# Kernel optimization log

Hardware: AMD Instinct MI355X
Metric: run time of the kernel (lower is better)

Reference implementation:

```python
import jax, jax.numpy as jnp
import numpy as np

EMBED_DIM = 1024
NUM_HEADS = 16
HEAD_DIM = EMBED_DIM // NUM_HEADS
B, S = 2, 2048


def setup_inputs() -> dict:
    key = jax.random.key(0)
    ks = jax.random.split(key, 11)
    sc = 1.0 / np.sqrt(EMBED_DIM)
    d = {
        'query': jax.random.normal(ks[0], (B, S, EMBED_DIM), jnp.float32),
        'key': jax.random.normal(ks[1], (B, S, EMBED_DIM), jnp.float32),
        'value': jax.random.normal(ks[2], (B, S, EMBED_DIM), jnp.float32),
        'Wq': jax.random.normal(ks[3], (EMBED_DIM, EMBED_DIM), jnp.float32) * sc,
        'bq': jnp.zeros((EMBED_DIM,), jnp.float32),
        'Wk': jax.random.normal(ks[4], (EMBED_DIM, EMBED_DIM), jnp.float32) * sc,
        'bk': jnp.zeros((EMBED_DIM,), jnp.float32),
        'Wv': jax.random.normal(ks[5], (EMBED_DIM, EMBED_DIM), jnp.float32) * sc,
        'bv': jnp.zeros((EMBED_DIM,), jnp.float32),
        'Wo': jax.random.normal(ks[6], (EMBED_DIM, EMBED_DIM), jnp.float32) * sc,
        'bo': jnp.zeros((EMBED_DIM,), jnp.float32),
    }
    return d


def reference(query, key, value, Wq, bq, Wk, bk, Wv, bv, Wo, bo):
    b, s, _ = query.shape
    scale = 1.0 / np.sqrt(HEAD_DIM)
    # projections: torch Linear is x @ W.T + b
    q = (query @ Wq.T + bq).reshape(b, s, NUM_HEADS, HEAD_DIM).transpose(0, 2, 1, 3)
    k = (key @ Wk.T + bk).reshape(b, s, NUM_HEADS, HEAD_DIM).transpose(0, 2, 1, 3)
    v = (value @ Wv.T + bv).reshape(b, s, NUM_HEADS, HEAD_DIM).transpose(0, 2, 1, 3)
    scores = jnp.einsum('bhqd,bhkd->bhqk', q, k) * scale  # [B,H,S,S]
    causal = jnp.triu(jnp.ones((s, s), bool), k=1)
    scores = jnp.where(causal, -jnp.inf, scores)
    attn = jax.nn.softmax(scores, axis=-1)
    out = jnp.einsum('bhqk,bhkd->bhqd', attn, v)
    out = out.transpose(0, 2, 1, 3).reshape(b, s, EMBED_DIM)
    out = out @ Wo.T + bo
    return out, attn
```

## Files before the change

### kernel.cpp

```cpp
#include <hip/hip_runtime.h>
#include <hip/hip_bf16.h>

#define BATCH  2
#define SEQ    2048
#define EMBED  1024
#define NHEADS 16
#define HDIM   64
#define SCALE  0.125f
#define S2     0.180336880f
#define MFIX   20.0f
#define PPITCH 72

typedef __attribute__((ext_vector_type(8))) short   short8;
typedef __attribute__((ext_vector_type(4))) float   floatx4;

#if __has_builtin(__builtin_amdgcn_exp2f)
#define EXP2(x) __builtin_amdgcn_exp2f(x)
#else
#define EXP2(x) exp2f(x)
#endif

#define GLOAD_LDS(g, l) __builtin_amdgcn_global_load_lds(                      \
    (const __attribute__((address_space(1))) void*)(const void*)(g),           \
    (__attribute__((address_space(3))) void*)(void*)(l), 16, 0, 0)

__device__ __forceinline__ float bf2f(unsigned short h) {
    union { unsigned int u; float f; } v; v.u = ((unsigned int)h) << 16; return v.f;
}
__device__ __forceinline__ unsigned short f2bf(float f) {
    union { float f; unsigned int u; } v; v.f = f;
    unsigned int r = v.u + 0x7FFF + ((v.u >> 16) & 1);
    return (unsigned short)(r >> 16);
}
__device__ __forceinline__ unsigned int pack2(float lo, float hi) {
    return (unsigned int)f2bf(lo) | ((unsigned int)f2bf(hi) << 16);
}

__device__ __forceinline__ void bar_lds() {
    __builtin_amdgcn_sched_barrier(0);
    asm volatile("s_waitcnt lgkmcnt(0)" ::: "memory");
    __builtin_amdgcn_s_barrier();
    __builtin_amdgcn_sched_barrier(0);
}

__global__ __launch_bounds__(256)
void cvt_bf16(const float* __restrict__ q,  const float* __restrict__ k,
              const float* __restrict__ v,  const float* __restrict__ wq,
              const float* __restrict__ wk, const float* __restrict__ wv,
              const float* __restrict__ wo,
              unsigned short* __restrict__ dq,  unsigned short* __restrict__ dk,
              unsigned short* __restrict__ dv,  unsigned short* __restrict__ dwq,
              unsigned short* __restrict__ dwk, unsigned short* __restrict__ dwv,
              unsigned short* __restrict__ dwo)
{
    const float* s; unsigned short* d; int n;
    switch (blockIdx.y) {
        case 0: s = q;  d = dq;  n = BATCH * SEQ * EMBED; break;
        case 1: s = k;  d = dk;  n = BATCH * SEQ * EMBED; break;
        case 2: s = v;  d = dv;  n = BATCH * SEQ * EMBED; break;
        case 3: s = wq; d = dwq; n = EMBED * EMBED; break;
        case 4: s = wk; d = dwk; n = EMBED * EMBED; break;
        case 5: s = wv; d = dwv; n = EMBED * EMBED; break;
        default: s = wo; d = dwo; n = EMBED * EMBED; break;
    }
    const int i = (blockIdx.x * 256 + threadIdx.x) * 8;
    if (i >= n) return;
    float4 f0 = ((const float4*)(s + i))[0];
    float4 f1 = ((const float4*)(s + i))[1];
    uint4 u = {pack2(f0.x, f0.y), pack2(f0.z, f0.w),
               pack2(f1.x, f1.y), pack2(f1.z, f1.w)};
    *(uint4*)(d + i) = u;
}

__device__ __forceinline__ void gemm_body(
    const unsigned short* __restrict__ A,
    const unsigned short* __restrict__ W,
    const float* __restrict__ bias,
    void* __restrict__ Cout, const int f32out,
    const int bx, const int by)
{
    constexpr int N = EMBED;
    constexpr int K = EMBED;

    __shared__ unsigned short As[128 * 64];
    __shared__ unsigned short Bs[128 * 64];

    const int t    = threadIdx.x;
    const int w    = t >> 6;
    const int lane = t & 63;
    const int lr   = lane & 15;
    const int quad = lane >> 4;
    const int wr   = w >> 1;
    const int wc   = w & 1;
    const int n0   = bx * 128;
    const int m0   = by * 128;

    size_t agoff[4], bgoff[4];
    #pragma unroll
    for (int i = 0; i < 4; ++i) {
        const int slot = i * 256 + t;
        const int row  = slot >> 3;
        const int g    = (slot & 7) ^ (row & 7);
        agoff[i] = (size_t)(m0 + row) * K + g * 8;
        bgoff[i] = (size_t)(n0 + row) * K + g * 8;
    }

    int aoff[4][2], boff[4][2];
    #pragma unroll
    for (int mb = 0; mb < 4; ++mb)
        #pragma unroll
        for (int s = 0; s < 2; ++s) {
            const int row = wr * 64 + mb * 16 + lr;
            aoff[mb][s] = row * 64 + (((s * 4 + quad) ^ (row & 7)) * 8);
        }
    #pragma unroll
    for (int nb = 0; nb < 4; ++nb)
        #pragma unroll
        for (int s = 0; s < 2; ++s) {
            const int row = wc * 64 + nb * 16 + lr;
            boff[nb][s] = row * 64 + (((s * 4 + quad) ^ (row & 7)) * 8);
        }

    floatx4 acc[4][4];
    #pragma unroll
    for (int mb = 0; mb < 4; ++mb)
        #pragma unroll
        for (int nb = 0; nb < 4; ++nb) acc[mb][nb] = (floatx4){0.f, 0.f, 0.f, 0.f};

    for (int k0 = 0; k0 < K; k0 += 64) {
        __syncthreads();
        #pragma unroll
        for (int i = 0; i < 4; ++i)
            GLOAD_LDS(A + agoff[i] + k0, &As[(i * 256 + w * 64) * 8]);
        #pragma unroll
        for (int i = 0; i < 4; ++i)
            GLOAD_LDS(W + bgoff[i] + k0, &Bs[(i * 256 + w * 64) * 8]);
        __syncthreads();

        #pragma unroll
        for (int s = 0; s < 2; ++s) {
            short8 av[4], bv[4];
            #pragma unroll
            for (int mb = 0; mb < 4; ++mb) av[mb] = *(const short8*)&As[aoff[mb][s]];
            #pragma unroll
            for (int nb = 0; nb < 4; ++nb) bv[nb] = *(const short8*)&Bs[boff[nb][s]];
            #pragma unroll
            for (int mb = 0; mb < 4; ++mb)
                #pragma unroll
                for (int nb = 0; nb < 4; ++nb)
                    acc[mb][nb] = __builtin_amdgcn_mfma_f32_16x16x32_bf16(av[mb], bv[nb], acc[mb][nb], 0, 0, 0);
        }
    }

    #pragma unroll
    for (int mb = 0; mb < 4; ++mb)
        #pragma unroll
        for (int nb = 0; nb < 4; ++nb) {
            const int col = n0 + wc * 64 + nb * 16 + lr;
            const float bv = bias[col];
            #pragma unroll
            for (int r = 0; r < 4; ++r) {
                const int row = m0 + wr * 64 + mb * 16 + quad * 4 + r;
                const float val = acc[mb][nb][r] + bv;
                if (f32out) ((float*)Cout)[(size_t)row * N + col] = val;
                else        ((unsigned short*)Cout)[(size_t)row * N + col] = f2bf(val);
            }
        }
}

__global__ __launch_bounds__(256)
void gemm_qkv(const unsigned short* __restrict__ xq, const unsigned short* __restrict__ xk,
              const unsigned short* __restrict__ xv,
              const unsigned short* __restrict__ wq, const unsigned short* __restrict__ wk,
              const unsigned short* __restrict__ wv,
              const float* __restrict__ bq, const float* __restrict__ bk,
              const float* __restrict__ bv,
              unsigned short* __restrict__ Qb, unsigned short* __restrict__ Kb,
              unsigned short* __restrict__ Vb)
{
    const unsigned short *A, *W; const float* bias; unsigned short* C;
    switch (blockIdx.z) {
        case 0:  A = xq; W = wq; bias = bq; C = Qb; break;
        case 1:  A = xk; W = wk; bias = bk; C = Kb; break;
        default: A = xv; W = wv; bias = bv; C = Vb; break;
    }
    gemm_body(A, W, bias, C, 0, blockIdx.x, blockIdx.y);
}

__global__ __launch_bounds__(256)
void gemm_out(const unsigned short* __restrict__ A, const unsigned short* __restrict__ W,
              const float* __restrict__ bias, float* __restrict__ Cout)
{
    gemm_body(A, W, bias, Cout, 1, blockIdx.x, blockIdx.y);
}

__global__ __launch_bounds__(256)
void attn_pass(const unsigned short* __restrict__ Qb,
               const unsigned short* __restrict__ Kb,
               const unsigned short* __restrict__ Vb,
               unsigned short* __restrict__ Pb,
               unsigned short* __restrict__ AO)
{
    __shared__ unsigned short Ks[2][64][PPITCH];
    __shared__ unsigned short Vt[2][64][PPITCH];
    __shared__ unsigned short Ps[64][PPITCH];
    __shared__ float          Linv[64];

    const int t    = threadIdx.x;
    const int w    = t >> 6;
    const int lane = t & 63;
    const int lr   = lane & 15;
    const int quad = lane >> 4;
    const int h    = blockIdx.y;
    const int b    = blockIdx.z;
    const int slot = (h >> 3) + 2 * b;
    const int qt   = (slot & 1) ? (SEQ / 64 - 1 - (int)blockIdx.x) : (int)blockIdx.x;
    const int q0   = qt * 64;
    const int srow = t >> 2;
    const int sseg = (t & 3) * 16;
    const int bh   = b * NHEADS + h;

    const size_t kvbase = (size_t)b * SEQ * EMBED + h * HDIM;

    const unsigned short* qrow = Qb + kvbase + (size_t)(q0 + w * 16 + lr) * EMBED + quad * 8;
    const short8 af0 = *(const short8*)(qrow);
    const short8 af1 = *(const short8*)(qrow + 32);

    const unsigned short* Krow = Kb + kvbase + (size_t)srow * EMBED + sseg;
    const unsigned short* Vrow = Vb + kvbase + (size_t)lane * EMBED;

    uint4 kA0, kA1, vA0, vA1;
    uint4 kB0, kB1, vB0, vB1;

    kA0 = ((const uint4*)Krow)[0];
    kA1 = ((const uint4*)Krow)[1];
    vA0 = *(const uint4*)(Vrow + w * 8);
    vA1 = *(const uint4*)(Vrow + (w + 4) * 8);
    *(uint4*)&Ks[0][srow][sseg]     = kA0;
    *(uint4*)&Ks[0][srow][sseg + 8] = kA1;
    {
        const unsigned short* p0 = (const unsigned short*)&vA0;
        const unsigned short* p1 = (const unsigned short*)&vA1;
        #pragma unroll
        for (int j = 0; j < 8; ++j) Vt[0][w * 8 + j][lane]       = p0[j];
        #pragma unroll
        for (int j = 0; j < 8; ++j) Vt[0][(w + 4) * 8 + j][lane] = p1[j];
    }
    if (qt > 0) {
        const unsigned short* kp = Krow + (size_t)64 * EMBED;
        kB0 = ((const uint4*)kp)[0];
        kB1 = ((const uint4*)kp)[1];
        vB0 = *(const uint4*)(Vrow + (size_t)64 * EMBED + w * 8);
        vB1 = *(const uint4*)(Vrow + (size_t)64 * EMBED + (w + 4) * 8);
    }
    bar_lds();

    float lsum[4];
    #pragma unroll
    for (int r = 0; r < 4; ++r) lsum[r] = 0.f;
    floatx4 of[4];
    #pragma unroll
    for (int i = 0; i < 4; ++i) of[i] = (floatx4){0.f, 0.f, 0.f, 0.f};

    unsigned short* pb_bh = Pb + (size_t)bh * SEQ * (SEQ * 2);
    const int rrow = lane >> 2;
    const int rseg = (lane & 3) * 16;

    for (int kt = 0; kt <= qt; ++kt) {
        const int c  = kt & 1;
        const int k0 = kt * 64;

        if (kt < qt) {
            if ((kt & 1) == 0) {
                *(uint4*)&Ks[c ^ 1][srow][sseg]     = kB0;
                *(uint4*)&Ks[c ^ 1][srow][sseg + 8] = kB1;
                const unsigned short* p0 = (const unsigned short*)&vB0;
                const unsigned short* p1 = (const unsigned short*)&vB1;
                #pragma unroll
                for (int j = 0; j < 8; ++j) Vt[c ^ 1][w * 8 + j][lane]       = p0[j];
                #pragma unroll
                for (int j = 0; j < 8; ++j) Vt[c ^ 1][(w + 4) * 8 + j][lane] = p1[j];
                if (kt + 2 <= qt) {
                    const unsigned short* kp = Krow + (size_t)(k0 + 128) * EMBED;
                    kA0 = ((const uint4*)kp)[0];
                    kA1 = ((const uint4*)kp)[1];
                    vA0 = *(const uint4*)(Vrow + (size_t)(k0 + 128) * EMBED + w * 8);
                    vA1 = *(const uint4*)(Vrow + (size_t)(k0 + 128) * EMBED + (w + 4) * 8);
                }
            } else {
                *(uint4*)&Ks[c ^ 1][srow][sseg]     = kA0;
                *(uint4*)&Ks[c ^ 1][srow][sseg + 8] = kA1;
                const unsigned short* p0 = (const unsigned short*)&vA0;
                const unsigned short* p1 = (const unsigned short*)&vA1;
                #pragma unroll
                for (int j = 0; j < 8; ++j) Vt[c ^ 1][w * 8 + j][lane]       = p0[j];
                #pragma unroll
                for (int j = 0; j < 8; ++j) Vt[c ^ 1][(w + 4) * 8 + j][lane] = p1[j];
                if (kt + 2 <= qt) {
                    const unsigned short* kp = Krow + (size_t)(k0 + 128) * EMBED;
                    kB0 = ((const uint4*)kp)[0];
                    kB1 = ((const uint4*)kp)[1];
                    vB0 = *(const uint4*)(Vrow + (size_t)(k0 + 128) * EMBED + w * 8);
                    vB1 = *(const uint4*)(Vrow + (size_t)(k0 + 128) * EMBED + (w + 4) * 8);
                }
            }
        }

        floatx4 sf[4];
        #pragma unroll
        for (int i = 0; i < 4; ++i) sf[i] = (floatx4){0.f, 0.f, 0.f, 0.f};
        #pragma unroll
        for (int nb = 0; nb < 4; ++nb) {
            short8 bf0 = *(const short8*)&Ks[c][nb * 16 + lr][quad * 8];
            sf[nb] = __builtin_amdgcn_mfma_f32_16x16x32_bf16(af0, bf0, sf[nb], 0, 0, 0);
        }
        #pragma unroll
        for (int nb = 0; nb < 4; ++nb) {
            short8 bf1 = *(const short8*)&Ks[c][nb * 16 + lr][32 + quad * 8];
            sf[nb] = __builtin_amdgcn_mfma_f32_16x16x32_bf16(af1, bf1, sf[nb], 0, 0, 0);
        }

        if (kt < qt) {
            #pragma unroll
            for (int nb = 0; nb < 4; ++nb)
                #pragma unroll
                for (int r = 0; r < 4; ++r) {
                    float p = EXP2(sf[nb][r] * S2 - MFIX);
                    lsum[r] += p;
                    Ps[w * 16 + quad * 4 + r][nb * 16 + lr] = f2bf(p);
                }
        } else {
            #pragma unroll
            for (int nb = 0; nb < 4; ++nb) {
                const int k = nb * 16 + lr;
                #pragma unroll
                for (int r = 0; r < 4; ++r) {
                    const int q = w * 16 + quad * 4 + r;
                    float p = 0.f;
                    if (k <= q) { p = EXP2(sf[nb][r] * S2 - MFIX); lsum[r] += p; }
                    Ps[w * 16 + quad * 4 + r][nb * 16 + lr] = f2bf(p);
                }
            }
        }

        {
            const unsigned short* ps = &Ps[w * 16 + rrow][rseg];
            unsigned short* op = pb_bh + (size_t)(q0 + w * 16 + rrow) * (SEQ * 2) + k0 + rseg;
            *(uint4*)op       = *(const uint4*)ps;
            *(uint4*)(op + 8) = *(const uint4*)(ps + 8);
        }

        #pragma unroll
        for (int ss = 0; ss < 2; ++ss) {
            short8 paf = *(const short8*)&Ps[w * 16 + lr][ss * 32 + quad * 8];
            #pragma unroll
            for (int nb = 0; nb < 4; ++nb) {
                short8 vf = *(const short8*)&Vt[c][nb * 16 + lr][ss * 32 + quad * 8];
                of[nb] = __builtin_amdgcn_mfma_f32_16x16x32_bf16(paf, vf, of[nb], 0, 0, 0);
            }
        }

        bar_lds();
    }

    float invl[4];
    #pragma unroll
    for (int r = 0; r < 4; ++r) {
        #pragma unroll
        for (int off = 1; off < 16; off <<= 1)
            lsum[r] += __shfl_xor(lsum[r], off, 64);
        invl[r] = 1.f / lsum[r];
    }
    if (lr == 0) {
        #pragma unroll
        for (int r = 0; r < 4; ++r)
            Linv[w * 16 + quad * 4 + r] = invl[r];
    }

    #pragma unroll
    for (int nb = 0; nb < 4; ++nb)
        #pragma unroll
        for (int r = 0; r < 4; ++r)
            Ps[w * 16 + quad * 4 + r][nb * 16 + lr] = f2bf(of[nb][r] * invl[r]);
    {
        unsigned short* ao = AO + (size_t)(b * SEQ + q0 + w * 16 + rrow) * EMBED + h * HDIM + rseg;
        *(uint4*)ao       = *(const uint4*)&Ps[w * 16 + rrow][rseg];
        *(uint4*)(ao + 8) = *(const uint4*)&Ps[w * 16 + rrow][rseg + 8];
    }

    __builtin_amdgcn_sched_barrier(0);
    asm volatile("s_waitcnt vmcnt(0) lgkmcnt(0)" ::: "memory");
    __builtin_amdgcn_sched_barrier(0);

    float* fb = ((float*)Pb) + (size_t)bh * SEQ * SEQ;
    const int qc = q0 + 64;
    for (int i = 0; i < 16; ++i) {
        const int q  = q0 + w * 16 + i;
        const float il = Linv[w * 16 + i];
        const unsigned short* src = pb_bh + (size_t)q * (SEQ * 2);
        float* dst = fb + (size_t)q * SEQ;

        uint4 rr[4];
        #pragma unroll
        for (int s = 0; s < 4; ++s) {
            const int cc = s * 512 + lane * 8;
            if (cc < qc) rr[s] = *(const uint4*)(src + cc);
        }
        #pragma unroll
        for (int s = 0; s < 4; ++s) {
            const int cc = s * 512 + lane * 8;
            if (cc < qc) {
                const unsigned short* u = (const unsigned short*)&rr[s];
                float4 f0 = {bf2f(u[0]) * il, bf2f(u[1]) * il, bf2f(u[2]) * il, bf2f(u[3]) * il};
                float4 f1 = {bf2f(u[4]) * il, bf2f(u[5]) * il, bf2f(u[6]) * il, bf2f(u[7]) * il};
                ((float4*)(dst + cc))[0] = f0;
                ((float4*)(dst + cc))[1] = f1;
            }
        }
    }
}

extern "C" void kernel_launch(void* const* d_in, const int* in_sizes, int n_in,
                              void* d_out, int out_size, void* d_ws, size_t ws_size,
                              hipStream_t stream)
{
    const float* query = (const float*)d_in[0];
    const float* key   = (const float*)d_in[1];
    const float* value = (const float*)d_in[2];
    const float* Wq    = (const float*)d_in[3];
    const float* bq    = (const float*)d_in[4];
    const float* Wk    = (const float*)d_in[5];
    const float* bk    = (const float*)d_in[6];
    const float* Wv    = (const float*)d_in[7];
    const float* bv    = (const float*)d_in[8];
    const float* Wo    = (const float*)d_in[9];
    const float* bo    = (const float*)d_in[10];

    float* out  = (float*)d_out;
    float* attn = out + (size_t)BATCH * SEQ * EMBED;

    const size_t tsz = (size_t)BATCH * SEQ * EMBED;
    const size_t wsz = (size_t)EMBED * EMBED;
    unsigned short* p = (unsigned short*)d_ws;
    unsigned short* xq  = p;  p += tsz;
    unsigned short* xk  = p;  p += tsz;
    unsigned short* xv  = p;  p += tsz;
    unsigned short* wq16 = p; p += wsz;
    unsigned short* wk16 = p; p += wsz;
    unsigned short* wv16 = p; p += wsz;
    unsigned short* wo16 = p; p += wsz;
    unsigned short* Qb  = p;  p += tsz;
    unsigned short* Kb  = p;  p += tsz;
    unsigned short* Vb  = p;  p += tsz;
    unsigned short* AO  = p;  p += tsz;

    const dim3 blk(256);

    cvt_bf16<<<dim3(2048, 7), blk, 0, stream>>>(query, key, value, Wq, Wk, Wv, Wo,
                                                xq, xk, xv, wq16, wk16, wv16, wo16);

    const dim3 gqkv(EMBED / 128, (BATCH * SEQ) / 128, 3);
    gemm_qkv<<<gqkv, blk, 0, stream>>>(xq, xk, xv, wq16, wk16, wv16,
                                       bq, bk, bv, Qb, Kb, Vb);

    attn_pass<<<dim3(SEQ / 64, NHEADS, BATCH), blk, 0, stream>>>(
        Qb, Kb, Vb, (unsigned short*)attn, AO);

    gemm_out<<<dim3(EMBED / 128, (BATCH * SEQ) / 128), blk, 0, stream>>>(AO, wo16, bo, out);
}
```

Before: 746.7 us.

## Recompute QK^T in a second pass to write normalized attn directly

Before, unnormalized bf16 probabilities were stored into the attn buffer during the flash loop, then read back, scaled by the row inverse sum and expanded to fp32. Now the first pass only accumulates row sums and the PV output. A second loop over K tiles recomputes the scores with MFMA and writes normalized fp32 probabilities straight to attn. This removes the bf16 scratch write and read-back round trip, at the cost of doubling the QK^T MFMA work and K tile loads. Upper-triangle entries are not written, so the code relies on attn being zeroed elsewhere.

```diff
diff --git a/kernel.cpp b/kernel.cpp
--- a/kernel.cpp
+++ b/kernel.cpp
@@ -198,13 +198,12 @@
 void attn_pass(const unsigned short* __restrict__ Qb,
                const unsigned short* __restrict__ Kb,
                const unsigned short* __restrict__ Vb,
-               unsigned short* __restrict__ Pb,
+               float* __restrict__ attn,
                unsigned short* __restrict__ AO)
 {
     __shared__ unsigned short Ks[2][64][PPITCH];
     __shared__ unsigned short Vt[2][64][PPITCH];
     __shared__ unsigned short Ps[64][PPITCH];
-    __shared__ float          Linv[64];
 
     const int t    = threadIdx.x;
     const int w    = t >> 6;
@@ -262,10 +261,6 @@
     #pragma unroll
     for (int i = 0; i < 4; ++i) of[i] = (floatx4){0.f, 0.f, 0.f, 0.f};
 
-    unsigned short* pb_bh = Pb + (size_t)bh * SEQ * (SEQ * 2);
-    const int rrow = lane >> 2;
-    const int rseg = (lane & 3) * 16;
-
     for (int kt = 0; kt <= qt; ++kt) {
         const int c  = kt & 1;
         const int k0 = kt * 64;
@@ -343,13 +338,6 @@
             }
         }
 
-        {
-            const unsigned short* ps = &Ps[w * 16 + rrow][rseg];
-            unsigned short* op = pb_bh + (size_t)(q0 + w * 16 + rrow) * (SEQ * 2) + k0 + rseg;
-            *(uint4*)op       = *(const uint4*)ps;
-            *(uint4*)(op + 8) = *(const uint4*)(ps + 8);
-        }
-
         #pragma unroll
         for (int ss = 0; ss < 2; ++ss) {
             short8 paf = *(const short8*)&Ps[w * 16 + lr][ss * 32 + quad * 8];
@@ -371,11 +359,6 @@
             lsum[r] += __shfl_xor(lsum[r], off, 64);
         invl[r] = 1.f / lsum[r];
     }
-    if (lr == 0) {
-        #pragma unroll
-        for (int r = 0; r < 4; ++r)
-            Linv[w * 16 + quad * 4 + r] = invl[r];
-    }
 
     #pragma unroll
     for (int nb = 0; nb < 4; ++nb)
@@ -383,40 +366,86 @@
         for (int r = 0; r < 4; ++r)
             Ps[w * 16 + quad * 4 + r][nb * 16 + lr] = f2bf(of[nb][r] * invl[r]);
     {
+        const int rrow = lane >> 2;
+        const int rseg = (lane & 3) * 16;
         unsigned short* ao = AO + (size_t)(b * SEQ + q0 + w * 16 + rrow) * EMBED + h * HDIM + rseg;
         *(uint4*)ao       = *(const uint4*)&Ps[w * 16 + rrow][rseg];
         *(uint4*)(ao + 8) = *(const uint4*)&Ps[w * 16 + rrow][rseg + 8];
     }
 
-    __builtin_amdgcn_sched_barrier(0);
-    asm volatile("s_waitcnt vmcnt(0) lgkmcnt(0)" ::: "memory");
-    __builtin_amdgcn_sched_barrier(0);
-
-    float* fb = ((float*)Pb) + (size_t)bh * SEQ * SEQ;
-    const int qc = q0 + 64;
-    for (int i = 0; i < 16; ++i) {
-        const int q  = q0 + w * 16 + i;
-        const float il = Linv[w * 16 + i];
-        const unsigned short* src = pb_bh + (size_t)q * (SEQ * 2);
-        float* dst = fb + (size_t)q * SEQ;
-
-        uint4 rr[4];
-        #pragma unroll
-        for (int s = 0; s < 4; ++s) {
-            const int cc = s * 512 + lane * 8;
-            if (cc < qc) rr[s] = *(const uint4*)(src + cc);
-        }
-        #pragma unroll
-        for (int s = 0; s < 4; ++s) {
-            const int cc = s * 512 + lane * 8;
-            if (cc < qc) {
-                const unsigned short* u = (const unsigned short*)&rr[s];
-                float4 f0 = {bf2f(u[0]) * il, bf2f(u[1]) * il, bf2f(u[2]) * il, bf2f(u[3]) * il};
-                float4 f1 = {bf2f(u[4]) * il, bf2f(u[5]) * il, bf2f(u[6]) * il, bf2f(u[7]) * il};
-                ((float4*)(dst + cc))[0] = f0;
-                ((float4*)(dst + cc))[1] = f1;
-            }
-        }
+    kA0 = ((const uint4*)Krow)[0];
+    kA1 = ((const uint4*)Krow)[1];
+    if (qt > 0) {
+        const unsigned short* kp = Krow + (size_t)64 * EMBED;
+        kB0 = ((const uint4*)kp)[0];
+        kB1 = ((const uint4*)kp)[1];
+    }
+    *(uint4*)&Ks[0][srow][sseg]     = kA0;
+    *(uint4*)&Ks[0][srow][sseg + 8] = kA1;
+    bar_lds();
+
+    float* fb = attn + (size_t)bh * SEQ * SEQ;
+    for (int kt = 0; kt <= qt; ++kt) {
+        const int c  = kt & 1;
+        const int k0 = kt * 64;
+
+        if (kt < qt) {
+            if ((kt & 1) == 0) {
+                *(uint4*)&Ks[c ^ 1][srow][sseg]     = kB0;
+                *(uint4*)&Ks[c ^ 1][srow][sseg + 8] = kB1;
+                if (kt + 2 <= qt) {
+                    const unsigned short* kp = Krow + (size_t)(k0 + 128) * EMBED;
+                    kA0 = ((const uint4*)kp)[0];
+                    kA1 = ((const uint4*)kp)[1];
+                }
+            } else {
+                *(uint4*)&Ks[c ^ 1][srow][sseg]     = kA0;
+                *(uint4*)&Ks[c ^ 1][srow][sseg + 8] = kA1;
+                if (kt + 2 <= qt) {
+                    const unsigned short* kp = Krow + (size_t)(k0 + 128) * EMBED;
+                    kB0 = ((const uint4*)kp)[0];
+                    kB1 = ((const uint4*)kp)[1];
+                }
+            }
+        }
+
+        floatx4 sf[4];
+        #pragma unroll
+        for (int i = 0; i < 4; ++i) sf[i] = (floatx4){0.f, 0.f, 0.f, 0.f};
+        #pragma unroll
+        for (int nb = 0; nb < 4; ++nb) {
+            short8 bf0 = *(const short8*)&Ks[c][nb * 16 + lr][quad * 8];
+            sf[nb] = __builtin_amdgcn_mfma_f32_16x16x32_bf16(af0, bf0, sf[nb], 0, 0, 0);
+        }
+        #pragma unroll
+        for (int nb = 0; nb < 4; ++nb) {
+            short8 bf1 = *(const short8*)&Ks[c][nb * 16 + lr][32 + quad * 8];
+            sf[nb] = __builtin_amdgcn_mfma_f32_16x16x32_bf16(af1, bf1, sf[nb], 0, 0, 0);
+        }
+
+        float* frow = fb + (size_t)(q0 + w * 16 + quad * 4) * SEQ + k0;
+        if (kt < qt) {
+            #pragma unroll
+            for (int nb = 0; nb < 4; ++nb)
+                #pragma unroll
+                for (int r = 0; r < 4; ++r)
+                    frow[(size_t)r * SEQ + nb * 16 + lr] =
+                        EXP2(sf[nb][r] * S2 - MFIX) * invl[r];
+        } else {
+            #pragma unroll
+            for (int nb = 0; nb < 4; ++nb) {
+                const int k = nb * 16 + lr;
+                #pragma unroll
+                for (int r = 0; r < 4; ++r) {
+                    const int q = w * 16 + quad * 4 + r;
+                    if (k <= q)
+                        frow[(size_t)r * SEQ + nb * 16 + lr] =
+                            EXP2(sf[nb][r] * S2 - MFIX) * invl[r];
+                }
+            }
+        }
+
+        bar_lds();
     }
 }
 
@@ -464,7 +493,7 @@
                                        bq, bk, bv, Qb, Kb, Vb);
 
     attn_pass<<<dim3(SEQ / 64, NHEADS, BATCH), blk, 0, stream>>>(
-        Qb, Kb, Vb, (unsigned short*)attn, AO);
+        Qb, Kb, Vb, attn, AO);
 
     gemm_out<<<dim3(EMBED / 128, (BATCH * SEQ) / 128), blk, 0, stream>>>(AO, wo16, bo, out);
 }
```

Result: faster. 721.0 us (-3.4%).
